# Kernel optimization log

Measured on AMD Instinct MI355X. Metric: run time of the kernel, lower is better.

## Reference

```python
import jax, jax.numpy as jnp
import numpy as np

B, T, S, D = 8, 32, 256, 1024


def setup_inputs() -> dict:
    key = jax.random.key(0)
    ks = jax.random.split(key, 10)
    scale = 1.0 / np.sqrt(D)
    return {
        "source1": jax.random.normal(ks[0], (B, T, D), jnp.float32),
        "source2": jax.random.normal(ks[1], (B, T, D), jnp.float32),
        "memory_bank": jax.random.normal(ks[2], (B, S, D), jnp.float32),
        "source_masks1": jnp.ones((B, T), jnp.float32),
        "source_masks2": jnp.ones((B, T), jnp.float32),
        "W_q1": jax.random.normal(ks[3], (D, D), jnp.float32) * scale,
        "b_q1": jnp.zeros((D,), jnp.float32),
        "W_q2": jax.random.normal(ks[4], (D, D), jnp.float32) * scale,
        "b_q2": jnp.zeros((D,), jnp.float32),
        "W_cate": jax.random.normal(ks[5], (2, 2 * D), jnp.float32) * scale,
        "b_cate": jnp.zeros((2,), jnp.float32),
        "W_v": jax.random.normal(ks[6], (D, D), jnp.float32) * scale,
    }


def reference(source1, source2, memory_bank, source_masks1, source_masks2,
              W_q1, b_q1, W_q2, b_q2, W_cate, b_cate, W_v):
    Bq, Tq, Dd = source1.shape
    # accumulate(): running prefix-mean over the segment axis, then mask.
    denom = jnp.arange(1, Tq + 1, dtype=source1.dtype)[None, :, None]
    s1 = (jnp.cumsum(source1, axis=1) / denom) * source_masks1[:, :, None]
    s2 = (jnp.cumsum(source2, axis=1) / denom) * source_masks2[:, :, None]
    # score(): gated attention scoring.
    q1 = s1 @ W_q1.T + b_q1  # [B,T,D]
    q2 = s2 @ W_q2.T + b_q2  # [B,T,D]
    # tanh gate broadcast over all (tgt, src) pairs -> [B,T,S,D]
    g = jnp.tanh(q1[:, :, None, :] + q2[:, :, None, :] + memory_bank[:, None, :, :])
    # sum_j (g @ W_v.T)[..., j] == g @ sum_j W_v[j, :]
    w_colsum = jnp.sum(W_v, axis=0)              # [D]
    sum_gate = g @ w_colsum                       # [B,T,S]
    # linear_cate(concat([h_s, sum_gate*h_s])) split into two halves
    pa = memory_bank @ W_cate[:, :Dd].T           # [B,S,2]
    pb = memory_bank @ W_cate[:, Dd:].T           # [B,S,2]
    out = pa[:, None, :, :] + sum_gate[..., None] * pb[:, None, :, :] + b_cate
    return out  # [B,T,S,2]
```

## Files before the change

kernel.cpp:

```cpp
#include <hip/hip_runtime.h>
#include <hip/hip_bf16.h>

#define Bb 8
#define Tt 32
#define Ss 256
#define Dd 1024
#define SCALE 2.885390081777927f

typedef short short8 __attribute__((ext_vector_type(8)));
typedef float floatx4 __attribute__((ext_vector_type(4)));

__device__ __forceinline__ unsigned short bf16b(float x) {
    __hip_bfloat16 h = __float2bfloat16(x);
    return *(unsigned short*)&h;
}

__device__ __forceinline__ float dot4(float4 a, float4 b) {
    return a.x * b.x + a.y * b.y + a.z * b.z + a.w * b.w;
}

__device__ __forceinline__ float sig2(float eqv, float emv, float w, float acc) {
    float e = eqv * emv;
    return fmaf(w, __builtin_amdgcn_rcpf(e + 1.f), acc);
}

__global__ __launch_bounds__(256) void prep_kernel(
        const float* __restrict__ src1, const float* __restrict__ src2,
        const float* __restrict__ m1, const float* __restrict__ m2,
        const float* __restrict__ W1, const float* __restrict__ W2,
        const float* __restrict__ Wv, const float* __restrict__ mem,
        const float* __restrict__ Wc,
        unsigned short* __restrict__ W1b, unsigned short* __restrict__ W2b,
        unsigned short* __restrict__ s1b, unsigned short* __restrict__ s2b,
        float* __restrict__ part, float* __restrict__ pab,
        float* __restrict__ em) {
    const int blk = blockIdx.x, tid = threadIdx.x;
    if (blk < 1024) {
        const int idx = blk * 256 + tid;
        float4 a = ((const float4*)W1)[idx];
        float4 b = ((const float4*)W2)[idx];
        ushort4 oa = { bf16b(a.x), bf16b(a.y), bf16b(a.z), bf16b(a.w) };
        ushort4 ob = { bf16b(b.x), bf16b(b.y), bf16b(b.z), bf16b(b.w) };
        ((ushort4*)W1b)[idx] = oa;
        ((ushort4*)W2b)[idx] = ob;
    } else if (blk < 1088) {
        const int bb = blk - 1024;
        const int db = bb & 3, jc = bb >> 2;
        const int d = db * 256 + tid;
        float a = 0.f;
        const int j0 = jc * 64;
        for (int j = 0; j < 64; j++)
            a += Wv[(size_t)(j0 + j) * Dd + d];
        part[jc * Dd + d] = a;
    } else if (blk < 1152) {
        const int idx = (blk - 1088) * 256 + tid;
        const int srcsel = idx >> 13;
        const int bd = idx & 8191;
        const int b = bd >> 10, d = bd & 1023;
        const float* sp = srcsel ? src2 : src1;
        const float* mp = srcsel ? m2 : m1;
        unsigned short* op = srcsel ? s2b : s1b;
        float a = 0.f;
        for (int t = 0; t < Tt; t++) {
            a += sp[(size_t)(b * Tt + t) * Dd + d];
            float inv = __builtin_amdgcn_rcpf((float)(t + 1));
            op[(size_t)(b * Tt + t) * Dd + d] = bf16b(a * inv * mp[b * Tt + t]);
        }
    } else {
        const int lane = tid & 63;
        const int bs = (blk - 1152) * 4 + (tid >> 6);
        const float4* mrow = (const float4*)mem + (size_t)bs * 256;
        float4* emr = (float4*)em + (size_t)bs * 256;
        const float4* Wc4 = (const float4*)Wc;
        float a0 = 0.f, a1 = 0.f, b0 = 0.f, b1 = 0.f;
        #pragma unroll
        for (int j = 0; j < 4; j++) {
            const int idx = j * 64 + lane;
            float4 m_ = mrow[idx];
            a0 += dot4(m_, Wc4[idx]);
            b0 += dot4(m_, Wc4[256 + idx]);
            a1 += dot4(m_, Wc4[512 + idx]);
            b1 += dot4(m_, Wc4[768 + idx]);
            float4 e4 = { __builtin_amdgcn_exp2f(SCALE * m_.x),
                          __builtin_amdgcn_exp2f(SCALE * m_.y),
                          __builtin_amdgcn_exp2f(SCALE * m_.z),
                          __builtin_amdgcn_exp2f(SCALE * m_.w) };
            emr[idx] = e4;
        }
        #pragma unroll
        for (int o = 32; o > 0; o >>= 1) {
            a0 += __shfl_xor(a0, o);
            a1 += __shfl_xor(a1, o);
            b0 += __shfl_xor(b0, o);
            b1 += __shfl_xor(b1, o);
        }
        if (lane == 0) {
            float4 r = { a0, a1, b0, b1 };
            ((float4*)pab)[bs] = r;
        }
    }
}

__global__ __launch_bounds__(64) void gemm_kernel(
        const unsigned short* __restrict__ s1b, const unsigned short* __restrict__ s2b,
        const unsigned short* __restrict__ W1b, const unsigned short* __restrict__ W2b,
        const float* __restrict__ bq1, const float* __restrict__ bq2,
        const float* __restrict__ part,
        float* __restrict__ qp, float* __restrict__ wsum) {
    const int blk = blockIdx.x;
    const int lane = threadIdx.x;
    if (blk >= 512) {
        const int d = (blk - 512) * 64 + lane;
        float a = 0.f;
        #pragma unroll
        for (int jc = 0; jc < 16; jc++)
            a += part[jc * Dd + d];
        wsum[d] = a;
        return;
    }
    const int m0 = (blk & 15) * 16;
    const int n0 = (blk >> 4) * 32;
    const int lm = lane & 15;
    const int quad = lane >> 4;

    floatx4 acc0 = {0.f, 0.f, 0.f, 0.f};
    floatx4 acc1 = {0.f, 0.f, 0.f, 0.f};
    const unsigned short* a1p = s1b + (size_t)(m0 + lm) * Dd;
    const unsigned short* a2p = s2b + (size_t)(m0 + lm) * Dd;
    const unsigned short* b1a = W1b + (size_t)(n0 + lm) * Dd;
    const unsigned short* b1b = W1b + (size_t)(n0 + 16 + lm) * Dd;
    const unsigned short* b2a = W2b + (size_t)(n0 + lm) * Dd;
    const unsigned short* b2b = W2b + (size_t)(n0 + 16 + lm) * Dd;

    #pragma unroll 2
    for (int k0 = 0; k0 < Dd; k0 += 32) {
        const int off = k0 + quad * 8;
        short8 a1 = *(const short8*)(a1p + off);
        short8 a2 = *(const short8*)(a2p + off);
        short8 vb1a = *(const short8*)(b1a + off);
        short8 vb2a = *(const short8*)(b2a + off);
        short8 vb1b = *(const short8*)(b1b + off);
        short8 vb2b = *(const short8*)(b2b + off);
        acc0 = __builtin_amdgcn_mfma_f32_16x16x32_bf16(a1, vb1a, acc0, 0, 0, 0);
        acc1 = __builtin_amdgcn_mfma_f32_16x16x32_bf16(a1, vb1b, acc1, 0, 0, 0);
        acc0 = __builtin_amdgcn_mfma_f32_16x16x32_bf16(a2, vb2a, acc0, 0, 0, 0);
        acc1 = __builtin_amdgcn_mfma_f32_16x16x32_bf16(a2, vb2b, acc1, 0, 0, 0);
    }

    const int na = n0 + lm, nb = n0 + 16 + lm;
    const float biasa = bq1[na] + bq2[na];
    const float biasb = bq1[nb] + bq2[nb];
    #pragma unroll
    for (int r = 0; r < 4; r++) {
        const int m = m0 + quad * 4 + r;
        qp[(size_t)m * Dd + na] = __builtin_amdgcn_exp2f(SCALE * (acc0[r] + biasa));
        qp[(size_t)m * Dd + nb] = __builtin_amdgcn_exp2f(SCALE * (acc1[r] + biasb));
    }
}

__global__ __launch_bounds__(256) void out_kernel(
        const float* __restrict__ eq, const float* __restrict__ em,
        const float* __restrict__ wsum, const float* __restrict__ pab,
        const float* __restrict__ bc, float* __restrict__ out) {
    __shared__ float em_s[4 * 1024];
    const int tid = threadIdx.x;
    const int wave = tid >> 6;
    const int lane = tid & 63;
    const int blk = blockIdx.x;
    const int sq = blk & 63, tg = (blk >> 6) & 1, b = blk >> 7;
    const int s0 = sq * 4;
    const int t0 = tg * 16 + wave * 4;
    const int bs0 = b * Ss + s0;

    {
        const float4* eg = (const float4*)em + (size_t)(bs0 + wave) * 256;
        float4* es = (float4*)em_s + wave * 256;
        #pragma unroll
        for (int k = 0; k < 4; k++)
            es[(tid & 63) + 64 * k] = eg[(tid & 63) + 64 * k];
    }

    const float4* q4 = (const float4*)eq;
    const float4* wsum4 = (const float4*)wsum;

    float4 wv[4];
    float Wl = 0.f;
    #pragma unroll
    for (int j = 0; j < 4; j++) {
        wv[j] = wsum4[j * 64 + lane];
        Wl += wv[j].x + wv[j].y + wv[j].z + wv[j].w;
    }
    #pragma unroll
    for (int o = 32; o > 0; o >>= 1) Wl += __shfl_xor(Wl, o);

    const float bc0 = bc[0], bc1 = bc[1];
    float C0[4], C1[4], D0[4], D1[4];
    #pragma unroll
    for (int si = 0; si < 4; si++) {
        float4 pv = ((const float4*)pab)[bs0 + si];
        C0[si] = pv.x + Wl * pv.z + bc0;
        C1[si] = pv.y + Wl * pv.w + bc1;
        D0[si] = 2.f * pv.z;
        D1[si] = 2.f * pv.w;
    }

    float p[4][4];
    #pragma unroll
    for (int ti = 0; ti < 4; ti++)
        #pragma unroll
        for (int si = 0; si < 4; si++) p[ti][si] = 0.f;

    __syncthreads();

    #pragma unroll
    for (int j = 0; j < 4; j++) {
        const int idx = j * 64 + lane;
        float4 emj[4], qj[4];
        #pragma unroll
        for (int si = 0; si < 4; si++)
            emj[si] = ((const float4*)em_s)[si * 256 + idx];
        #pragma unroll
        for (int ti = 0; ti < 4; ti++)
            qj[ti] = q4[(size_t)(b * Tt + t0 + ti) * 256 + idx];
        const float4 w_ = wv[j];
        #pragma unroll
        for (int ti = 0; ti < 4; ti++) {
            #pragma unroll
            for (int si = 0; si < 4; si++) {
                float acc = p[ti][si];
                acc = sig2(qj[ti].x, emj[si].x, w_.x, acc);
                acc = sig2(qj[ti].y, emj[si].y, w_.y, acc);
                acc = sig2(qj[ti].z, emj[si].z, w_.z, acc);
                acc = sig2(qj[ti].w, emj[si].w, w_.w, acc);
                p[ti][si] = acc;
            }
        }
    }

    #pragma unroll
    for (int ti = 0; ti < 4; ti++)
        #pragma unroll
        for (int si = 0; si < 4; si++) {
            float v = p[ti][si];
            #pragma unroll
            for (int o = 32; o > 0; o >>= 1) v += __shfl_xor(v, o);
            p[ti][si] = v;
        }

    if (lane == 0) {
        #pragma unroll
        for (int ti = 0; ti < 4; ti++) {
            const size_t rowo = ((size_t)(b * Tt + t0 + ti) * Ss + s0) * 2;
            #pragma unroll
            for (int si = 0; si < 4; si++) {
                float2 o2 = { C0[si] - D0[si] * p[ti][si],
                              C1[si] - D1[si] * p[ti][si] };
                *(float2*)(out + rowo + si * 2) = o2;
            }
        }
    }
}

extern "C" void kernel_launch(void* const* d_in, const int* in_sizes, int n_in,
                              void* d_out, int out_size, void* d_ws, size_t ws_size,
                              hipStream_t stream) {
    const float* src1 = (const float*)d_in[0];
    const float* src2 = (const float*)d_in[1];
    const float* mem  = (const float*)d_in[2];
    const float* m1   = (const float*)d_in[3];
    const float* m2   = (const float*)d_in[4];
    const float* Wq1  = (const float*)d_in[5];
    const float* bq1  = (const float*)d_in[6];
    const float* Wq2  = (const float*)d_in[7];
    const float* bq2  = (const float*)d_in[8];
    const float* Wc   = (const float*)d_in[9];
    const float* bc   = (const float*)d_in[10];
    const float* Wv   = (const float*)d_in[11];
    float* out = (float*)d_out;

    char* ws = (char*)d_ws;
    unsigned short* s1b = (unsigned short*)(ws);
    unsigned short* s2b = (unsigned short*)(ws + (512u << 10));
    unsigned short* W1b = (unsigned short*)(ws + (1u << 20));
    unsigned short* W2b = (unsigned short*)(ws + (3u << 20));
    float* qp   = (float*)(ws + (5u << 20));
    float* wsum = (float*)(ws + (6u << 20));
    float* part = (float*)(ws + (6u << 20) + 4096);
    float* pab  = (float*)(ws + (6u << 20) + 4096 + 65536);
    float* em   = (float*)(ws + (7u << 20));

    prep_kernel<<<1664, 256, 0, stream>>>(src1, src2, m1, m2, Wq1, Wq2, Wv,
                                          mem, Wc, W1b, W2b, s1b, s2b,
                                          part, pab, em);
    gemm_kernel<<<528, 64, 0, stream>>>(s1b, s2b, W1b, W2b, bq1, bq2, part,
                                        qp, wsum);
    out_kernel<<<1024, 256, 0, stream>>>(qp, em, wsum, pab, bc, out);
}
```

Baseline: 119.6 us.

## Compute exp(memory) inline in out kernel and move cate projection into gemm launch

Stops materialising the exponentiated memory bank in a workspace buffer. The out kernel now reads the raw memory bank and applies exp2 while filling shared memory, which removes an 8 MB write and re-read. The per-row W_cate projection moves from the prep kernel into 2048 extra 64-thread blocks of the gemm launch, so prep gets shorter. The cost is recomputing exp for each memory row in every out block that loads it (two t-groups share a row) and more small blocks in the gemm grid.

```diff
diff --git a/kernel.cpp b/kernel.cpp
--- a/kernel.cpp
+++ b/kernel.cpp
@@ -28,12 +28,10 @@
         const float* __restrict__ src1, const float* __restrict__ src2,
         const float* __restrict__ m1, const float* __restrict__ m2,
         const float* __restrict__ W1, const float* __restrict__ W2,
-        const float* __restrict__ Wv, const float* __restrict__ mem,
-        const float* __restrict__ Wc,
+        const float* __restrict__ Wv,
         unsigned short* __restrict__ W1b, unsigned short* __restrict__ W2b,
         unsigned short* __restrict__ s1b, unsigned short* __restrict__ s2b,
-        float* __restrict__ part, float* __restrict__ pab,
-        float* __restrict__ em) {
+        float* __restrict__ part) {
     const int blk = blockIdx.x, tid = threadIdx.x;
     if (blk < 1024) {
         const int idx = blk * 256 + tid;
@@ -52,7 +50,7 @@
         for (int j = 0; j < 64; j++)
             a += Wv[(size_t)(j0 + j) * Dd + d];
         part[jc * Dd + d] = a;
-    } else if (blk < 1152) {
+    } else {
         const int idx = (blk - 1088) * 256 + tid;
         const int srcsel = idx >> 13;
         const int bd = idx & 8191;
@@ -66,11 +64,22 @@
             float inv = __builtin_amdgcn_rcpf((float)(t + 1));
             op[(size_t)(b * Tt + t) * Dd + d] = bf16b(a * inv * mp[b * Tt + t]);
         }
-    } else {
-        const int lane = tid & 63;
-        const int bs = (blk - 1152) * 4 + (tid >> 6);
+    }
+}
+
+__global__ __launch_bounds__(64) void gemm_kernel(
+        const unsigned short* __restrict__ s1b, const unsigned short* __restrict__ s2b,
+        const unsigned short* __restrict__ W1b, const unsigned short* __restrict__ W2b,
+        const float* __restrict__ bq1, const float* __restrict__ bq2,
+        const float* __restrict__ part, const float* __restrict__ mem,
+        const float* __restrict__ Wc,
+        float* __restrict__ qp, float* __restrict__ wsum,
+        float* __restrict__ pab) {
+    const int blk = blockIdx.x;
+    const int lane = threadIdx.x;
+    if (blk >= 528) {
+        const int bs = blk - 528;
         const float4* mrow = (const float4*)mem + (size_t)bs * 256;
-        float4* emr = (float4*)em + (size_t)bs * 256;
         const float4* Wc4 = (const float4*)Wc;
         float a0 = 0.f, a1 = 0.f, b0 = 0.f, b1 = 0.f;
         #pragma unroll
@@ -81,11 +90,6 @@
             b0 += dot4(m_, Wc4[256 + idx]);
             a1 += dot4(m_, Wc4[512 + idx]);
             b1 += dot4(m_, Wc4[768 + idx]);
-            float4 e4 = { __builtin_amdgcn_exp2f(SCALE * m_.x),
-                          __builtin_amdgcn_exp2f(SCALE * m_.y),
-                          __builtin_amdgcn_exp2f(SCALE * m_.z),
-                          __builtin_amdgcn_exp2f(SCALE * m_.w) };
-            emr[idx] = e4;
         }
         #pragma unroll
         for (int o = 32; o > 0; o >>= 1) {
@@ -98,17 +102,8 @@
             float4 r = { a0, a1, b0, b1 };
             ((float4*)pab)[bs] = r;
         }
-    }
-}
-
-__global__ __launch_bounds__(64) void gemm_kernel(
-        const unsigned short* __restrict__ s1b, const unsigned short* __restrict__ s2b,
-        const unsigned short* __restrict__ W1b, const unsigned short* __restrict__ W2b,
-        const float* __restrict__ bq1, const float* __restrict__ bq2,
-        const float* __restrict__ part,
-        float* __restrict__ qp, float* __restrict__ wsum) {
-    const int blk = blockIdx.x;
-    const int lane = threadIdx.x;
+        return;
+    }
     if (blk >= 512) {
         const int d = (blk - 512) * 64 + lane;
         float a = 0.f;
@@ -159,7 +154,7 @@
 }
 
 __global__ __launch_bounds__(256) void out_kernel(
-        const float* __restrict__ eq, const float* __restrict__ em,
+        const float* __restrict__ eq, const float* __restrict__ mem,
         const float* __restrict__ wsum, const float* __restrict__ pab,
         const float* __restrict__ bc, float* __restrict__ out) {
     __shared__ float em_s[4 * 1024];
@@ -173,11 +168,17 @@
     const int bs0 = b * Ss + s0;
 
     {
-        const float4* eg = (const float4*)em + (size_t)(bs0 + wave) * 256;
+        const float4* mg = (const float4*)mem + (size_t)(bs0 + wave) * 256;
         float4* es = (float4*)em_s + wave * 256;
         #pragma unroll
-        for (int k = 0; k < 4; k++)
-            es[(tid & 63) + 64 * k] = eg[(tid & 63) + 64 * k];
+        for (int k = 0; k < 4; k++) {
+            float4 m_ = mg[lane + 64 * k];
+            float4 e4 = { __builtin_amdgcn_exp2f(SCALE * m_.x),
+                          __builtin_amdgcn_exp2f(SCALE * m_.y),
+                          __builtin_amdgcn_exp2f(SCALE * m_.z),
+                          __builtin_amdgcn_exp2f(SCALE * m_.w) };
+            es[lane + 64 * k] = e4;
+        }
     }
 
     const float4* q4 = (const float4*)eq;
@@ -287,12 +288,10 @@
     float* wsum = (float*)(ws + (6u << 20));
     float* part = (float*)(ws + (6u << 20) + 4096);
     float* pab  = (float*)(ws + (6u << 20) + 4096 + 65536);
-    float* em   = (float*)(ws + (7u << 20));
-
-    prep_kernel<<<1664, 256, 0, stream>>>(src1, src2, m1, m2, Wq1, Wq2, Wv,
-                                          mem, Wc, W1b, W2b, s1b, s2b,
-                                          part, pab, em);
-    gemm_kernel<<<528, 64, 0, stream>>>(s1b, s2b, W1b, W2b, bq1, bq2, part,
-                                        qp, wsum);
-    out_kernel<<<1024, 256, 0, stream>>>(qp, em, wsum, pab, bc, out);
-}
+
+    prep_kernel<<<1152, 256, 0, stream>>>(src1, src2, m1, m2, Wq1, Wq2, Wv,
+                                          W1b, W2b, s1b, s2b, part);
+    gemm_kernel<<<2576, 64, 0, stream>>>(s1b, s2b, W1b, W2b, bq1, bq2, part,
+                                         mem, Wc, qp, wsum, pab);
+    out_kernel<<<1024, 256, 0, stream>>>(qp, mem, wsum, pab, bc, out);
+}
```

After: 121.8 us. Within noise of the previous version (+1.9%).
